# Kernel optimization log

Hardware: AMD Instinct MI355X
Metric: run time of the kernel (lower is better)

Reference implementation:

```python
import jax, jax.numpy as jnp
import numpy as np

N = 50000      # nodes
E = 800000     # edges (avg degree 16)
F = 6          # input node features
C = 64         # conv_hidden_channels
M = 256        # mlp_hidden_channels
NCLS = 24      # num_classes
EPS = 1e-5     # BatchNorm eps


def _bn(h, g, b):
    # BatchNorm1d in training mode: biased batch stats over the batch axis
    mu = h.mean(axis=0)
    var = ((h - mu) ** 2).mean(axis=0)
    return g * (h - mu) * jax.lax.rsqrt(var + EPS) + b


def _block(x, W, b, g, beta):
    # Lin -> ReLU -> BN  (one MLP block)
    return _bn(jax.nn.relu(x @ W + b), g, beta)


def _edge_conv(x, src, dst, Wa, ba, ga, bea, Wb, bb, gb, beb):
    # EdgeConv: message = MLP([x_i, x_j - x_i]), max-aggregated onto target i
    xi = x[dst]                                   # [E, d]
    xj = x[src]                                   # [E, d]
    e = jnp.concatenate([xi, xj - xi], axis=-1)   # [E, 2d]
    h = _block(_block(e, Wa, ba, ga, bea), Wb, bb, gb, beb)  # [E, C]
    agg = jax.ops.segment_max(h, dst, num_segments=N)        # [N, C]
    return jnp.where(jnp.isfinite(agg), agg, 0.0)  # zero-fill isolated nodes


def setup_inputs() -> dict:
    key = jax.random.key(0)
    ks = jax.random.split(key, 12)

    def w(k, shape, fan_in):
        return jax.random.normal(k, shape, jnp.float32) * (1.0 / np.sqrt(fan_in))

    z = lambda *s: jnp.zeros(s, jnp.float32)
    o = lambda *s: jnp.ones(s, jnp.float32)

    x = jax.random.normal(ks[0], (N, F), jnp.float32)
    edge_index = jax.random.randint(ks[1], (2, E), 0, N, jnp.int32)

    return {
        "x": x,
        # conv1 MLP: Lin(2F,C)+BN, Lin(C,C)+BN
        "W1a": w(ks[2], (2 * F, C), 2 * F), "b1a": z(C), "g1a": o(C), "be1a": z(C),
        "W1b": w(ks[3], (C, C), C),         "b1b": z(C), "g1b": o(C), "be1b": z(C),
        # conv2/conv3 stacked: Lin(2C,C)+BN, Lin(C,C)+BN
        "Wa": w(ks[4], (2, 2 * C, C), 2 * C), "ba": z(2, C), "ga": o(2, C), "bea": z(2, C),
        "Wb": w(ks[5], (2, C, C), C),         "bb": z(2, C), "gb": o(2, C), "beb": z(2, C),
        # lin1: Lin(3C, M)+BN
        "Wl": w(ks[6], (3 * C, M), 3 * C), "bl": z(M), "gl": o(M), "bel": z(M),
        # head: Lin(M, M/4)+BN, Lin(M/4, M/8)+BN, Lin(M/8, NCLS)
        "Wm1": w(ks[7], (M, M // 4), M),      "bm1": z(M // 4), "gm1": o(M // 4), "bem1": z(M // 4),
        "Wm2": w(ks[8], (M // 4, M // 8), M // 4), "bm2": z(M // 8), "gm2": o(M // 8), "bem2": z(M // 8),
        "Wo": w(ks[9], (M // 8, NCLS), M // 8), "bo": z(NCLS),
        "edge_index": edge_index,
    }


def reference(x, W1a, b1a, g1a, be1a, W1b, b1b, g1b, be1b,
              Wa, ba, ga, bea, Wb, bb, gb, beb,
              Wl, bl, gl, bel,
              Wm1, bm1, gm1, bem1, Wm2, bm2, gm2, bem2,
              Wo, bo, edge_index):
    src, dst = edge_index[0], edge_index[1]
    x1 = _edge_conv(x,  src, dst, W1a, b1a, g1a, be1a, W1b, b1b, g1b, be1b)
    x2 = _edge_conv(x1, src, dst, Wa[0], ba[0], ga[0], bea[0], Wb[0], bb[0], gb[0], beb[0])
    x3 = _edge_conv(x2, src, dst, Wa[1], ba[1], ga[1], bea[1], Wb[1], bb[1], gb[1], beb[1])
    h = _block(jnp.concatenate([x1, x2, x3], axis=-1), Wl, bl, gl, bel)
    h = _block(h, Wm1, bm1, gm1, bem1)   # Dropout is identity (eval)
    h = _block(h, Wm2, bm2, gm2, bem2)   # Dropout is identity (eval)
    logits = h @ Wo + bo
    return jax.nn.log_softmax(logits, axis=1)
```

## Files before the change

### kernel.cpp

```cpp
#include <hip/hip_runtime.h>
#include <hip/hip_bf16.h>

#define EPS 1e-5f
typedef unsigned short bfr;
typedef unsigned short hfr;
typedef _Float16 h2v __attribute__((ext_vector_type(2)));
typedef _Float16 f16x8 __attribute__((ext_vector_type(8)));
typedef float f32x4 __attribute__((ext_vector_type(4)));

#if defined(__has_builtin)
#if __has_builtin(__builtin_amdgcn_fdot2)
#define HAS_FDOT2 1
#endif
#endif

static inline int cdiv(int a, int b){ return (a + b - 1) / b; }
static inline int imin(int a, int b){ return a < b ? a : b; }

__device__ __forceinline__ float bf2f(bfr u){ return __uint_as_float((unsigned)u << 16); }
__device__ __forceinline__ bfr f2bf(float f){
  unsigned u = __float_as_uint(f);
  u += 0x7fffu + ((u >> 16) & 1u);
  return (bfr)(u >> 16);
}
__device__ __forceinline__ unsigned pack2bf(float a, float b){
  return (unsigned)f2bf(a) | ((unsigned)f2bf(b) << 16);
}
__device__ __forceinline__ float h2f(hfr u){ _Float16 h; __builtin_memcpy(&h, &u, 2); return (float)h; }
__device__ __forceinline__ hfr f2h(float f){ _Float16 h = (_Float16)f; hfr u; __builtin_memcpy(&u, &h, 2); return u; }
__device__ __forceinline__ unsigned pack2h(float a, float b){
  return (unsigned)f2h(a) | ((unsigned)f2h(b) << 16);
}
__device__ __forceinline__ h2v u2h2(unsigned u){ h2v r; __builtin_memcpy(&r, &u, 4); return r; }
__device__ __forceinline__ unsigned h22u(h2v h){ unsigned u; __builtin_memcpy(&u, &h, 4); return u; }
__device__ __forceinline__ float dot2(h2v a, h2v b, float c){
#ifdef HAS_FDOT2
  return __builtin_amdgcn_fdot2(a, b, c, false);
#else
  return c + (float)a.x * (float)b.x + (float)a.y * (float)b.y;
#endif
}

__global__ __launch_bounds__(256) void detect_kernel(const bfr* __restrict__ xr, int nwords, int* __restrict__ flag){
  int i = threadIdx.x;
  int bad = 0;
  if (i < nwords){
    bfr lo = xr[2 * i];
    int e = (lo >> 7) & 0xFF;
    bool plausible = ((lo & 0x7FFF) == 0) || (e >= 97 && e <= 157);
    bad = plausible ? 0 : 1;
  }
  __shared__ int s[256];
  s[threadIdx.x] = bad; __syncthreads();
  for (int st = 128; st; st >>= 1){
    if (threadIdx.x < st) s[threadIdx.x] += s[threadIdx.x + st];
    __syncthreads();
  }
  if (threadIdx.x == 0) *flag = (s[0] > 32) ? 1 : 0;
}

#define NPAR 31
struct ParamPtrs { const void* p[NPAR]; };
struct ParamOfs  { int off[NPAR + 1]; };

__global__ __launch_bounds__(256) void acvt_batch_kernel(ParamPtrs pp, ParamOfs po,
                                                         float* __restrict__ out, int total,
                                                         const int* __restrict__ flag){
  int g = blockIdx.x * 256 + threadIdx.x;
  if (g >= total) return;
  int isf = *flag;
  int t = 0;
  while (po.off[t + 1] <= g) ++t;
  int i = g - po.off[t];
  out[g] = isf ? ((const float*)pp.p[t])[i] : bf2f(((const bfr*)pp.p[t])[i]);
}

__global__ __launch_bounds__(256) void deg_kernel(const int* __restrict__ dst, int* __restrict__ deg, int E){
  int e = blockIdx.x * 256 + threadIdx.x;
  if (e < E) atomicAdd(&deg[dst[e]], 1);
}

__global__ __launch_bounds__(256) void scan1_kernel(const int* __restrict__ deg, int* __restrict__ locoff,
                                                    int* __restrict__ bsum, int N){
  __shared__ int s[256];
  int i = blockIdx.x * 256 + threadIdx.x;
  int v = (i < N) ? deg[i] : 0;
  s[threadIdx.x] = v; __syncthreads();
  for (int st = 1; st < 256; st <<= 1){
    int u = (threadIdx.x >= st) ? s[threadIdx.x - st] : 0;
    __syncthreads();
    s[threadIdx.x] += u;
    __syncthreads();
  }
  if (i < N) locoff[i] = s[threadIdx.x] - v;
  if (threadIdx.x == 255) bsum[blockIdx.x] = s[255];
}

__global__ __launch_bounds__(256) void scan2_kernel(int* __restrict__ bsum, int nb){
  __shared__ int s[256];
  const int t = threadIdx.x;
  int carry = 0;
  for (int base = 0; base < nb; base += 256){
    int v = (base + t < nb) ? bsum[base + t] : 0;
    s[t] = v; __syncthreads();
    for (int st = 1; st < 256; st <<= 1){
      int u = (t >= st) ? s[t - st] : 0;
      __syncthreads();
      s[t] += u;
      __syncthreads();
    }
    if (base + t < nb) bsum[base + t] = carry + s[t] - v;
    carry += s[255];
    __syncthreads();
  }
}

__global__ __launch_bounds__(256) void scan3_kernel(const int* __restrict__ locoff, const int* __restrict__ bsum,
                                                    int* __restrict__ row_off, int* __restrict__ cur,
                                                    int N, int E){
  int i = blockIdx.x * 256 + threadIdx.x;
  if (i < N){
    int v = locoff[i] + bsum[blockIdx.x];
    row_off[i] = v; cur[i] = v;
  }
  if (i == 0) row_off[N] = E;
}

__global__ __launch_bounds__(256) void scatter_kernel(const int* __restrict__ src, const int* __restrict__ dst,
                                                      int* __restrict__ cur, int* __restrict__ ssrc, int E){
  int e = blockIdx.x * 256 + threadIdx.x;
  if (e < E){
    int d = dst[e];
    int p = atomicAdd(&cur[d], 1);
    ssrc[p] = src[e];
  }
}

template<bool FIRST>
__global__ __launch_bounds__(256) void gemmPQ_kernel(const void* __restrict__ Av, int lda,
                                                     const float* __restrict__ Wa, int d,
                                                     const float* __restrict__ ba,
                                                     hfr* __restrict__ P, hfr* __restrict__ Q, int N){
  __shared__ unsigned WsU[64 * 64];
  const int y = blockIdx.y;
  const int tot = d * 64;
  if (FIRST){
    float* Ws = (float*)WsU;
    for (int i = threadIdx.x; i < tot; i += 256)
      Ws[i] = y ? Wa[tot + i] : (Wa[i] - Wa[tot + i]);
  } else {
    for (int i = threadIdx.x; i < 32 * 64; i += 256){
      int p = i >> 6, c = i & 63;
      int i0 = (2 * p) * 64 + c, i1 = (2 * p + 1) * 64 + c;
      float w0 = y ? Wa[tot + i0] : (Wa[i0] - Wa[tot + i0]);
      float w1 = y ? Wa[tot + i1] : (Wa[i1] - Wa[tot + i1]);
      WsU[i] = pack2h(w0, w1);
    }
  }
  __syncthreads();
  const int row = blockIdx.x * 256 + threadIdx.x;
  if (row >= N) return;
  float acc[64];
#pragma unroll
  for (int c = 0; c < 64; ++c) acc[c] = 0.f;
  if (FIRST){
    const float* Ws = (const float*)WsU;
    const float* Af = (const float*)Av + (size_t)row * lda;
    for (int k = 0; k < d; ++k){
      float a = Af[k];
      const float* wr = Ws + k * 64;
#pragma unroll
      for (int c4 = 0; c4 < 16; ++c4){
        float4 w = *(const float4*)(wr + 4 * c4);
        acc[4*c4+0] += a * w.x; acc[4*c4+1] += a * w.y;
        acc[4*c4+2] += a * w.z; acc[4*c4+3] += a * w.w;
      }
    }
  } else {
    const hfr* Ah = (const hfr*)Av + (size_t)row * lda;
#pragma unroll
    for (int k8 = 0; k8 < 8; ++k8){
      uint4 av = *(const uint4*)(Ah + k8 * 8);
      unsigned pr[4] = {av.x, av.y, av.z, av.w};
#pragma unroll
      for (int pi = 0; pi < 4; ++pi){
        h2v ap = u2h2(pr[pi]);
        const unsigned* wr = WsU + (k8 * 4 + pi) * 64;
#pragma unroll
        for (int c = 0; c < 64; ++c) acc[c] = dot2(ap, u2h2(wr[c]), acc[c]);
      }
    }
  }
  if (!y){
#pragma unroll
    for (int c = 0; c < 64; ++c) acc[c] += ba[c];
  }
  unsigned p[32];
#pragma unroll
  for (int c = 0; c < 64; c += 2) p[c / 2] = pack2h(acc[c], acc[c + 1]);
  hfr* outp = (y ? Q : P) + (size_t)row * 64;
  uint4* op = (uint4*)outp;
#pragma unroll
  for (int i = 0; i < 8; ++i) op[i] = make_uint4(p[4*i], p[4*i+1], p[4*i+2], p[4*i+3]);
}

template<int NOUT, int KSTEPS, bool FOLD, bool PQ, bool STATS>
__global__ __launch_bounds__(256) void mgemm_kernel(const hfr* __restrict__ Ah, int lda,
                                                    const float* __restrict__ Wp0, const float* __restrict__ Wm0, int ldw,
                                                    const float* __restrict__ bias0,
                                                    const float* __restrict__ stats, float cntInv,
                                                    const float* __restrict__ g, const float* __restrict__ be,
                                                    hfr* __restrict__ Ov0, hfr* __restrict__ Ov1, int ldo,
                                                    float* __restrict__ statsOut, int statC,
                                                    int nrows, int relu){
  constexpr int K  = KSTEPS * 32;
  constexpr int KP = K + 8;
  constexpr int NT = NOUT / 16;
  __shared__ __align__(16) _Float16 W2T[NOUT * KP];
  __shared__ __align__(16) _Float16 etile[4][16][NOUT + 8];
  __shared__ float aS[FOLD ? K : 1], bbS[FOLD ? K : 1], bsum[FOLD ? 256 : 1];
  __shared__ float bfull[NOUT];
  __shared__ float sred[STATS ? 4 * NOUT : 1], qred[STATS ? 4 * NOUT : 1];
  const int tid = threadIdx.x;
  const int lane = tid & 63;
  const int wib = tid >> 6;
  const float* Wp = Wp0;
  const float* Wm = Wm0;
  const float* bias = bias0;
  hfr* Ov = Ov0;
  int colbase = blockIdx.y * NOUT;
  if (PQ){
    colbase = 0;
    if (blockIdx.y == 1){ Wp = Wp0 + (size_t)K * ldw; Wm = nullptr; bias = nullptr; Ov = Ov1; }
    else { Wm = Wp0 + (size_t)K * ldw; }
  }

  if (FOLD){
    for (int k = tid; k < K; k += 256){
      float mu = stats[k] * cntInv;
      float var = stats[K + k] * cntInv - mu * mu;
      float ai = g[k] * rsqrtf(var + EPS);
      aS[k] = ai; bbS[k] = be[k] - ai * mu;
    }
    __syncthreads();
  }
  for (int i = tid; i < K * NOUT; i += 256){
    int k = i / NOUT, c = i - k * NOUT;
    float w = Wp[(size_t)k * ldw + colbase + c];
    if (Wm) w -= Wm[(size_t)k * ldw + colbase + c];
    if (FOLD) w *= aS[k];
    W2T[c * KP + k] = (_Float16)w;
  }
  if (FOLD){
    constexpr int parts = 256 / NOUT;
    int c = tid % NOUT, p = tid / NOUT;
    float s = 0.f;
    for (int k = p; k < K; k += parts) s += bbS[k] * Wp[(size_t)k * ldw + colbase + c];
    bsum[p * NOUT + c] = s;
    __syncthreads();
    if (tid < NOUT){
      float t = bias[colbase + tid];
#pragma unroll
      for (int pp = 0; pp < parts; ++pp) t += bsum[pp * NOUT + tid];
      bfull[tid] = t;
    }
  } else {
    if (tid < NOUT) bfull[tid] = bias ? bias[colbase + tid] : 0.f;
  }
  __syncthreads();

  f16x8 Bf[KSTEPS][NT];
#pragma unroll
  for (int s = 0; s < KSTEPS; ++s)
#pragma unroll
    for (int t = 0; t < NT; ++t)
      Bf[s][t] = *(const f16x8*)&W2T[(t * 16 + (lane & 15)) * KP + s * 32 + (lane >> 4) * 8];
  float bc[NT];
#pragma unroll
  for (int t = 0; t < NT; ++t) bc[t] = bfull[t * 16 + (lane & 15)];

  float ssum[STATS ? NT : 1], qsum[STATS ? NT : 1];
  if (STATS){
#pragma unroll
    for (int t = 0; t < (STATS ? NT : 1); ++t){ ssum[t] = 0.f; qsum[t] = 0.f; }
  }
  const int lq2 = lane >> 4;

  const int ntiles = (nrows + 63) >> 6;
  for (int tile = blockIdx.x; tile < ntiles; tile += gridDim.x){
    const int r0 = tile * 64 + wib * 16;
    const int rowA = min(r0 + (lane & 15), nrows - 1);
    const hfr* Ap = Ah + (size_t)rowA * lda + (lane >> 4) * 8;
    f32x4 acc[NT];
#pragma unroll
    for (int t = 0; t < NT; ++t) acc[t] = (f32x4){bc[t], bc[t], bc[t], bc[t]};
#pragma unroll
    for (int s = 0; s < KSTEPS; ++s){
      f16x8 Af = *(const f16x8*)(Ap + s * 32);
#pragma unroll
      for (int t = 0; t < NT; ++t)
        acc[t] = __builtin_amdgcn_mfma_f32_16x16x32_f16(Af, Bf[s][t], acc[t], 0, 0, 0);
    }
    const bool fullTile = (r0 + 16 <= nrows);
#pragma unroll
    for (int t = 0; t < NT; ++t){
#pragma unroll
      for (int r = 0; r < 4; ++r){
        float v = acc[t][r];
        v = relu ? fmaxf(v, 0.f) : v;
        if (STATS){
          float vs = v;
          if (!fullTile) vs = ((r0 + lq2 * 4 + r) < nrows) ? vs : 0.f;
          ssum[t] += vs;
          qsum[t]  = fmaf(vs, vs, qsum[t]);
        }
        etile[wib][lq2 * 4 + r][t * 16 + (lane & 15)] = (_Float16)v;
      }
    }
    if (NOUT == 64){
#pragma unroll
      for (int h = 0; h < 2; ++h){
        int rl = h * 8 + (lane >> 3);
        int ch = lane & 7;
        uint4 vv = *(const uint4*)&etile[wib][rl][ch * 8];
        int rg = r0 + rl;
        if (rg < nrows) *(uint4*)(Ov + (size_t)rg * ldo + colbase + ch * 8) = vv;
      }
    } else {
      int rl = lane >> 2;
      int ch = lane & 3;
      uint4 vv = *(const uint4*)&etile[wib][rl][ch * 8];
      int rg = r0 + rl;
      if (rg < nrows) *(uint4*)(Ov + (size_t)rg * ldo + colbase + ch * 8) = vv;
    }
  }

  if (STATS){
#pragma unroll
    for (int t = 0; t < NT; ++t){
      float s = ssum[t], q = qsum[t];
      s += __shfl_xor(s, 16, 64); s += __shfl_xor(s, 32, 64);
      q += __shfl_xor(q, 16, 64); q += __shfl_xor(q, 32, 64);
      if (lq2 == 0){ sred[wib * NOUT + t * 16 + lane] = s; qred[wib * NOUT + t * 16 + lane] = q; }
    }
    __syncthreads();
    if (tid < NOUT){
      float s = sred[tid] + sred[NOUT + tid] + sred[2 * NOUT + tid] + sred[3 * NOUT + tid];
      float q = qred[tid] + qred[NOUT + tid] + qred[2 * NOUT + tid] + qred[3 * NOUT + tid];
      atomicAdd(&statsOut[colbase + tid], s);
      atomicAdd(&statsOut[statC + colbase + tid], q);
    }
  }
}

__global__ __launch_bounds__(256) void passA_kernel(const hfr* __restrict__ P, const hfr* __restrict__ Q,
                                                    const int* __restrict__ ssrc, const int* __restrict__ row_off,
                                                    float* __restrict__ stats, hfr* __restrict__ h1, int N){
  const int tid = threadIdx.x;
  const int lane = tid & 63;
  const int wib = tid >> 6;
  const int er0 = lane >> 3;
  const int ck = lane & 7;
  const int wid = (blockIdx.x * 256 + tid) >> 6;
  const int nw = (gridDim.x * 256) >> 6;
  const _Float16 z16 = (_Float16)0;
  float s8[8], q8[8];
#pragma unroll
  for (int j = 0; j < 8; ++j){ s8[j] = 0.f; q8[j] = 0.f; }
  for (int n = wid; n < N; n += nw){
    const int e0 = row_off[n], e1 = row_off[n + 1];
    if (e0 >= e1) continue;
    uint4 pv4 = ((const uint4*)(P + (size_t)n * 64))[ck];
    h2v pp0 = u2h2(pv4.x), pp1 = u2h2(pv4.y), pp2 = u2h2(pv4.z), pp3 = u2h2(pv4.w);
    const int lim = e1 - 1;
    for (int eb = e0; eb < e1; eb += 16){
      int sv = ssrc[min(eb + (lane & 15), lim)];
#pragma unroll
      for (int h = 0; h < 2; ++h){
        int er = h * 8 + er0;
        int ge = eb + er;
        int sj = __shfl(sv, er, 64);
        uint4 qv = *((const uint4*)(Q + (size_t)sj * 64) + ck);
        h2v s0 = u2h2(qv.x) + pp0;
        h2v s1 = u2h2(qv.y) + pp1;
        h2v s2 = u2h2(qv.z) + pp2;
        h2v s3 = u2h2(qv.w) + pp3;
        s0.x = (s0.x < z16) ? z16 : s0.x; s0.y = (s0.y < z16) ? z16 : s0.y;
        s1.x = (s1.x < z16) ? z16 : s1.x; s1.y = (s1.y < z16) ? z16 : s1.y;
        s2.x = (s2.x < z16) ? z16 : s2.x; s2.y = (s2.y < z16) ? z16 : s2.y;
        s3.x = (s3.x < z16) ? z16 : s3.x; s3.y = (s3.y < z16) ? z16 : s3.y;
        if (ge < e1){
          *(uint4*)(h1 + (size_t)ge * 64 + ck * 8) = make_uint4(h22u(s0), h22u(s1), h22u(s2), h22u(s3));
          float v;
          v = (float)s0.x; s8[0] += v; q8[0] = fmaf(v, v, q8[0]);
          v = (float)s0.y; s8[1] += v; q8[1] = fmaf(v, v, q8[1]);
          v = (float)s1.x; s8[2] += v; q8[2] = fmaf(v, v, q8[2]);
          v = (float)s1.y; s8[3] += v; q8[3] = fmaf(v, v, q8[3]);
          v = (float)s2.x; s8[4] += v; q8[4] = fmaf(v, v, q8[4]);
          v = (float)s2.y; s8[5] += v; q8[5] = fmaf(v, v, q8[5]);
          v = (float)s3.x; s8[6] += v; q8[6] = fmaf(v, v, q8[6]);
          v = (float)s3.y; s8[7] += v; q8[7] = fmaf(v, v, q8[7]);
        }
      }
    }
  }
#pragma unroll
  for (int j = 0; j < 8; ++j){
    float s = s8[j], q = q8[j];
    s += __shfl_xor(s, 8, 64);  q += __shfl_xor(q, 8, 64);
    s += __shfl_xor(s, 16, 64); q += __shfl_xor(q, 16, 64);
    s += __shfl_xor(s, 32, 64); q += __shfl_xor(q, 32, 64);
    s8[j] = s; q8[j] = q;
  }
  __shared__ float ls[4][64], lq[4][64];
  if (lane < 8){
#pragma unroll
    for (int j = 0; j < 8; ++j){ ls[wib][lane * 8 + j] = s8[j]; lq[wib][lane * 8 + j] = q8[j]; }
  }
  __syncthreads();
  if (tid < 64){
    atomicAdd(&stats[tid], ls[0][tid] + ls[1][tid] + ls[2][tid] + ls[3][tid]);
  } else if (tid < 128){
    int c = tid - 64;
    atomicAdd(&stats[64 + c], lq[0][c] + lq[1][c] + lq[2][c] + lq[3][c]);
  }
}

__global__ __launch_bounds__(256) void passBC_kernel(const hfr* __restrict__ h1,
                                                     const int* __restrict__ row_off,
                                                     const float* __restrict__ statsIn, float Einv,
                                                     const float* __restrict__ g1, const float* __restrict__ be1,
                                                     const float* __restrict__ Wb, const float* __restrict__ bn,
                                                     float* __restrict__ agg, float* __restrict__ statsOut, int N){
  __shared__ __align__(16) _Float16 W2T[64 * 72];
  __shared__ float aS[64], bbS[64], b2S[64], bsum[256], qsum[256];
  const int tid = threadIdx.x;
  const int lane = tid & 63;
  if (tid < 64){
    float mu = statsIn[tid] * Einv;
    float var = statsIn[64 + tid] * Einv - mu * mu;
    float ai = g1[tid] * rsqrtf(var + EPS);
    aS[tid] = ai; bbS[tid] = be1[tid] - ai * mu;
  }
  __syncthreads();
  for (int i = tid; i < 4096; i += 256){
    int c = i >> 6, k = i & 63;
    W2T[c * 72 + k] = (_Float16)(aS[k] * Wb[(size_t)k * 64 + c]);
  }
  {
    int c = tid & 63, p = tid >> 6;
    float s = 0.f;
    for (int k = p; k < 64; k += 4) s += bbS[k] * Wb[(size_t)k * 64 + c];
    bsum[p * 64 + c] = s;
  }
  __syncthreads();
  if (tid < 64) b2S[tid] = bn[tid] + bsum[tid] + bsum[64 + tid] + bsum[128 + tid] + bsum[192 + tid];
  __syncthreads();
  f16x8 Bf[4][2];
#pragma unroll
  for (int t = 0; t < 4; ++t)
#pragma unroll
    for (int h = 0; h < 2; ++h){
      int c = t * 16 + (lane & 15);
      Bf[t][h] = *(const f16x8*)&W2T[c * 72 + h * 32 + (lane >> 4) * 8];
    }
  float bc[4];
#pragma unroll
  for (int t = 0; t < 4; ++t) bc[t] = b2S[t * 16 + (lane & 15)];
  const int wid = (blockIdx.x * 256 + tid) >> 6;
  const int nw = (gridDim.x * 256) >> 6;
  float sumT[4] = {0.f,0.f,0.f,0.f}, sqT[4] = {0.f,0.f,0.f,0.f};
  for (int n = wid; n < N; n += nw){
    const int e0 = row_off[n], e1 = row_off[n + 1];
    if (e0 >= e1) continue;
    float mxT[4] = {0.f,0.f,0.f,0.f};
    for (int eb = e0; eb < e1; eb += 16){
      const hfr* ap = h1 + (size_t)(eb + (lane & 15)) * 64 + (lane >> 4) * 8;
      f16x8 A0 = *(const f16x8*)ap;
      f16x8 A1 = *(const f16x8*)(ap + 32);
#pragma unroll
      for (int t = 0; t < 4; ++t){
        f32x4 Cv = {bc[t], bc[t], bc[t], bc[t]};
        Cv = __builtin_amdgcn_mfma_f32_16x16x32_f16(A0, Bf[t][0], Cv, 0, 0, 0);
        Cv = __builtin_amdgcn_mfma_f32_16x16x32_f16(A1, Bf[t][1], Cv, 0, 0, 0);
#pragma unroll
        for (int r = 0; r < 4; ++r){
          int rowi = (lane >> 4) * 4 + r;
          float v = fmaxf(Cv[r], 0.f);
          v = ((eb + rowi) < e1) ? v : 0.f;
          mxT[t] = fmaxf(mxT[t], v);
          sumT[t] += v;
          sqT[t]  = fmaf(v, v, sqT[t]);
        }
      }
    }
#pragma unroll
    for (int t = 0; t < 4; ++t){
      float m = mxT[t];
      m = fmaxf(m, __shfl_xor(m, 16, 64));
      m = fmaxf(m, __shfl_xor(m, 32, 64));
      mxT[t] = m;
    }
    float outv = (lane < 16) ? mxT[0] : (lane < 32) ? mxT[1] : (lane < 48) ? mxT[2] : mxT[3];
    agg[(size_t)n * 64 + lane] = outv;
  }
#pragma unroll
  for (int t = 0; t < 4; ++t){
    float s = sumT[t], q = sqT[t];
    s += __shfl_xor(s, 16, 64); s += __shfl_xor(s, 32, 64);
    q += __shfl_xor(q, 16, 64); q += __shfl_xor(q, 32, 64);
    sumT[t] = s; sqT[t] = q;
  }
  float ssel = (lane < 16) ? sumT[0] : (lane < 32) ? sumT[1] : (lane < 48) ? sumT[2] : sumT[3];
  float qsel = (lane < 16) ? sqT[0]  : (lane < 32) ? sqT[1]  : (lane < 48) ? sqT[2]  : sqT[3];
  bsum[tid] = ssel; qsum[tid] = qsel;
  __syncthreads();
  if (tid < 64){
    atomicAdd(&statsOut[tid], bsum[tid] + bsum[64 + tid] + bsum[128 + tid] + bsum[192 + tid]);
  } else if (tid < 128){
    int c = tid - 64;
    atomicAdd(&statsOut[64 + c], qsum[c] + qsum[64 + c] + qsum[128 + c] + qsum[192 + c]);
  }
}

__global__ __launch_bounds__(256) void fixup_kernel(const float* __restrict__ agg, const int* __restrict__ deg,
                                                    const float* __restrict__ stats, float cntInv,
                                                    const float* __restrict__ g, const float* __restrict__ be,
                                                    hfr* __restrict__ xout, int ldx, int N){
  int t = blockIdx.x * 256 + threadIdx.x;
  if (t >= N * 64) return;
  int n = t >> 6, c = t & 63;
  float mu = stats[c] * cntInv;
  float var = stats[64 + c] * cntInv - mu * mu;
  float a = g[c] * rsqrtf(var + EPS);
  float b = be[c] - a * mu;
  float v = 0.f;
  if (deg[n] > 0) v = a * agg[t] + b;
  xout[(size_t)n * ldx + c] = f2h(v);
}

__global__ __launch_bounds__(256) void head_kernel(const hfr* __restrict__ u2,
                                                   const float* __restrict__ stats, float cntInv,
                                                   const float* __restrict__ g, const float* __restrict__ be,
                                                   const float* __restrict__ Wo, const float* __restrict__ bo,
                                                   void* __restrict__ out, int N, const int* __restrict__ flag){
  __shared__ float Ws[32 * 24];
  __shared__ float bs[24];
  __shared__ float aS[32], bbS[32];
  const int tid = threadIdx.x;
  if (tid < 32){
    float mu = stats[tid] * cntInv;
    float var = stats[32 + tid] * cntInv - mu * mu;
    float ai = g[tid] * rsqrtf(var + EPS);
    aS[tid] = ai; bbS[tid] = be[tid] - ai * mu;
  }
  __syncthreads();
  for (int i = tid; i < 32 * 24; i += 256){
    int k = i / 24, c = i - 24 * k;
    Ws[i] = aS[k] * Wo[(size_t)k * 24 + c];
  }
  if (tid < 24){
    float t = bo[tid];
    for (int k = 0; k < 32; ++k) t += bbS[k] * Wo[(size_t)k * 24 + tid];
    bs[tid] = t;
  }
  __syncthreads();
  int r = blockIdx.x * 256 + tid;
  if (r >= N) return;
  int isf = *flag;
  float l[24];
#pragma unroll
  for (int c = 0; c < 24; ++c) l[c] = bs[c];
  const hfr* up = u2 + (size_t)r * 32;
#pragma unroll
  for (int k = 0; k < 32; ++k){
    float v = h2f(up[k]);
#pragma unroll
    for (int c = 0; c < 24; ++c) l[c] += v * Ws[k * 24 + c];
  }
  float m = l[0];
#pragma unroll
  for (int c = 1; c < 24; ++c) m = fmaxf(m, l[c]);
  float s = 0.f;
#pragma unroll
  for (int c = 0; c < 24; ++c) s += expf(l[c] - m);
  float lse = m + logf(s);
  if (isf){
    float4* op = (float4*)((float*)out + (size_t)r * 24);
#pragma unroll
    for (int i = 0; i < 6; ++i)
      op[i] = make_float4(l[4*i] - lse, l[4*i+1] - lse, l[4*i+2] - lse, l[4*i+3] - lse);
  } else {
    unsigned p[12];
#pragma unroll
    for (int c = 0; c < 24; c += 2) p[c / 2] = pack2bf(l[c] - lse, l[c + 1] - lse);
    uint4* op = (uint4*)((bfr*)out + (size_t)r * 24);
#pragma unroll
    for (int i = 0; i < 3; ++i) op[i] = make_uint4(p[4*i], p[4*i+1], p[4*i+2], p[4*i+3]);
  }
}

extern "C" void kernel_launch(void* const* d_in, const int* in_sizes, int n_in,
                              void* d_out, int out_size, void* d_ws, size_t ws_size,
                              hipStream_t stream){
  const int N = in_sizes[0] / 6;
  const int E = in_sizes[31] / 2;
  const int* edge = (const int*)d_in[31];
  const int* src = edge;
  const int* dst = edge + E;

  size_t off = 0; char* basep = (char*)d_ws;
  auto alloc = [&](size_t bytes) -> void* {
    void* p = basep + off;
    off = (off + bytes + 255) & ~(size_t)255;
    return p;
  };
  float* stA  = (float*)alloc(1472 * 4);
  float* stN1 = stA + 768;
  float* stN2 = stA + 1280;
  float* stN3 = stA + 1408;
  int*   flag = (int*)  alloc(4);
  int*   deg  = (int*)  alloc((size_t)N * 4);
  int*   rowo = (int*)  alloc((size_t)(N + 1) * 4);
  int*   cur  = (int*)  alloc((size_t)N * 4);
  int*   loco = (int*)  alloc((size_t)N * 4);
  int*   bsc  = (int*)  alloc(1024 * 4);
  int*   ssrc = (int*)  alloc((size_t)E * 4);

  ParamPtrs pp; ParamOfs po;
  int hoff[32]; int total = 0;
  for (int s = 0; s < NPAR; ++s){
    int idx = (s < 30) ? (s + 1) : 0;
    pp.p[s] = d_in[idx];
    po.off[s] = total;
    hoff[idx] = total;
    total += in_sizes[idx];
  }
  po.off[NPAR] = total;
  float* pf = (float*)alloc((size_t)total * 4);

  hfr*   P    = (hfr*)  alloc((size_t)N * 64 * 2);
  hfr*   Qb   = (hfr*)  alloc((size_t)N * 64 * 2);
  float* agg  = (float*)alloc((size_t)N * 64 * 4);
  hfr*   xcat = (hfr*)  alloc((size_t)N * 192 * 2);
  hfr*   h1   = (hfr*)  alloc((size_t)(E + 16) * 64 * 2);
  hfr* u_l = (hfr*)P;
  hfr* u1  = xcat;
  hfr* u2  = xcat + (size_t)N * 64;
  (void)ws_size; (void)n_in; (void)out_size;

  dim3 B(256);
  detect_kernel<<<1, B, 0, stream>>>((const bfr*)d_in[0], 256, flag);
  acvt_batch_kernel<<<cdiv(total, 256), B, 0, stream>>>(pp, po, pf, total, flag);

  hipMemsetAsync(stA, 0, 1472 * 4, stream);
  hipMemsetAsync(deg, 0, (size_t)N * 4, stream);
  hipMemsetAsync(h1 + (size_t)E * 64, 0, 16 * 64 * 2, stream);
  deg_kernel<<<cdiv(E, 256), B, 0, stream>>>(dst, deg, E);
  const int NBn = cdiv(N, 256);
  scan1_kernel<<<NBn, B, 0, stream>>>(deg, loco, bsc, N);
  scan2_kernel<<<1, B, 0, stream>>>(bsc, NBn);
  scan3_kernel<<<NBn, B, 0, stream>>>(loco, bsc, rowo, cur, N, E);
  scatter_kernel<<<cdiv(E, 256), B, 0, stream>>>(src, dst, cur, ssrc, E);

  const int NB = cdiv(N, 256);
  const int ntiles = cdiv(N, 64);
  const int GWA = 1024, GWB = 1024;
  const float Einv = 1.f / (float)E;
  for (int k = 0; k < 3; ++k){
    const float *Wa_k, *ba_k, *ga_k, *bea_k, *Wb_k, *bb_k, *gb_k, *beb_k;
    if (k == 0){
      Wa_k = pf + hoff[1]; ba_k = pf + hoff[2]; ga_k = pf + hoff[3]; bea_k = pf + hoff[4];
      Wb_k = pf + hoff[5]; bb_k = pf + hoff[6]; gb_k = pf + hoff[7]; beb_k = pf + hoff[8];
    } else {
      int kk = k - 1;
      Wa_k = pf + hoff[9]  + (size_t)kk * 128 * 64;
      ba_k = pf + hoff[10] + kk * 64;
      ga_k = pf + hoff[11] + kk * 64;
      bea_k= pf + hoff[12] + kk * 64;
      Wb_k = pf + hoff[13] + (size_t)kk * 64 * 64;
      bb_k = pf + hoff[14] + kk * 64;
      gb_k = pf + hoff[15] + kk * 64;
      beb_k= pf + hoff[16] + kk * 64;
    }
    float* st1 = stA + k * 256;
    float* st2 = st1 + 128;
    if (k == 0){
      gemmPQ_kernel<true><<<dim3(NB, 2), B, 0, stream>>>(pf + hoff[0], 6, Wa_k, 6, ba_k, P, Qb, N);
    } else {
      mgemm_kernel<64, 2, false, true, false><<<dim3(imin(ntiles, 1024), 2), B, 0, stream>>>(
          xcat + (size_t)(k - 1) * 64, 192, Wa_k, nullptr, 64, ba_k,
          nullptr, 0.f, nullptr, nullptr, P, Qb, 64, nullptr, 0, N, 0);
    }
    passA_kernel<<<GWA, B, 0, stream>>>(P, Qb, ssrc, rowo, st1, h1, N);
    passBC_kernel<<<GWB, B, 0, stream>>>(h1, rowo, st1, Einv, ga_k, bea_k, Wb_k, bb_k,
                                         agg, st2, N);
    fixup_kernel<<<cdiv(N * 64, 256), B, 0, stream>>>(agg, deg, st2, Einv, gb_k, beb_k,
                                                      xcat + (size_t)k * 64, 192, N);
  }

  mgemm_kernel<64, 6, false, false, true><<<dim3(imin(ntiles, 256), 4), B, 0, stream>>>(
      xcat, 192, pf + hoff[17], nullptr, 256, pf + hoff[18],
      nullptr, 0.f, nullptr, nullptr, u_l, nullptr, 256, stN1, 256, N, 1);
  mgemm_kernel<32, 8, true, false, true><<<dim3(imin(ntiles, 512), 2), B, 0, stream>>>(
      u_l, 256, pf + hoff[21], nullptr, 64, pf + hoff[22],
      stN1, 1.f / (float)N, pf + hoff[19], pf + hoff[20], u1, nullptr, 64, stN2, 64, N, 1);
  mgemm_kernel<32, 2, true, false, true><<<dim3(imin(ntiles, 1024), 1), B, 0, stream>>>(
      u1, 64, pf + hoff[25], nullptr, 32, pf + hoff[26],
      stN2, 1.f / (float)N, pf + hoff[23], pf + hoff[24], u2, nullptr, 32, stN3, 32, N, 1);
  head_kernel<<<cdiv(N, 256), B, 0, stream>>>(u2, stN3, 1.f / (float)N, pf + hoff[27], pf + hoff[28],
                                              pf + hoff[29], pf + hoff[30], d_out, N, flag);
  (void)NB;
}
```

Measured before the change: 723.5 us.

## Fuse scan passes, merge P/Q GEMM into one 128-wide pass, vectorize fixup

Drops the single-block scan2 kernel; each scan3 block now computes its own carry by reducing the preceding block sums. The P and Q projections for conv2/3 are computed in one mgemm launch with NOUT=128, so the A tile is read once instead of twice, and the output is split between the two buffers on write. The fixup kernel now precomputes the BN scale and shift per block in shared memory and handles four channels per thread with float4 loads and packed half stores. These target launch overhead and redundant memory traffic, in exchange for redundant carry sums in scan3 and more weight registers in the wider GEMM.

```diff
diff --git a/kernel.cpp b/kernel.cpp
--- a/kernel.cpp
+++ b/kernel.cpp
@@ -96,31 +96,26 @@
   if (threadIdx.x == 255) bsum[blockIdx.x] = s[255];
 }
 
-__global__ __launch_bounds__(256) void scan2_kernel(int* __restrict__ bsum, int nb){
-  __shared__ int s[256];
-  const int t = threadIdx.x;
-  int carry = 0;
-  for (int base = 0; base < nb; base += 256){
-    int v = (base + t < nb) ? bsum[base + t] : 0;
-    s[t] = v; __syncthreads();
-    for (int st = 1; st < 256; st <<= 1){
-      int u = (t >= st) ? s[t - st] : 0;
-      __syncthreads();
-      s[t] += u;
-      __syncthreads();
-    }
-    if (base + t < nb) bsum[base + t] = carry + s[t] - v;
-    carry += s[255];
-    __syncthreads();
-  }
-}
-
 __global__ __launch_bounds__(256) void scan3_kernel(const int* __restrict__ locoff, const int* __restrict__ bsum,
                                                     int* __restrict__ row_off, int* __restrict__ cur,
                                                     int N, int E){
-  int i = blockIdx.x * 256 + threadIdx.x;
+  __shared__ int s[256];
+  const int t = threadIdx.x;
+  const int bid = blockIdx.x;
+  int acc = 0;
+  for (int base = 0; base < bid; base += 256){
+    int idx = base + t;
+    acc += (idx < bid) ? bsum[idx] : 0;
+  }
+  s[t] = acc; __syncthreads();
+  for (int st = 128; st; st >>= 1){
+    if (t < st) s[t] += s[t + st];
+    __syncthreads();
+  }
+  const int carry = s[0];
+  int i = bid * 256 + t;
   if (i < N){
-    int v = locoff[i] + bsum[blockIdx.x];
+    int v = locoff[i] + carry;
     row_off[i] = v; cur[i] = v;
   }
   if (i == 0) row_off[N] = E;
@@ -204,7 +199,7 @@
   for (int i = 0; i < 8; ++i) op[i] = make_uint4(p[4*i], p[4*i+1], p[4*i+2], p[4*i+3]);
 }
 
-template<int NOUT, int KSTEPS, bool FOLD, bool PQ, bool STATS>
+template<int NOUT, int KSTEPS, bool FOLD, bool PQ, bool STATS, bool PQ2>
 __global__ __launch_bounds__(256) void mgemm_kernel(const hfr* __restrict__ Ah, int lda,
                                                     const float* __restrict__ Wp0, const float* __restrict__ Wm0, int ldw,
                                                     const float* __restrict__ bias0,
@@ -234,6 +229,7 @@
     if (blockIdx.y == 1){ Wp = Wp0 + (size_t)K * ldw; Wm = nullptr; bias = nullptr; Ov = Ov1; }
     else { Wm = Wp0 + (size_t)K * ldw; }
   }
+  if (PQ2) colbase = 0;
 
   if (FOLD){
     for (int k = tid; k < K; k += 256){
@@ -246,8 +242,14 @@
   }
   for (int i = tid; i < K * NOUT; i += 256){
     int k = i / NOUT, c = i - k * NOUT;
-    float w = Wp[(size_t)k * ldw + colbase + c];
-    if (Wm) w -= Wm[(size_t)k * ldw + colbase + c];
+    float w;
+    if (PQ2){
+      w = (c < 64) ? (Wp[(size_t)k * ldw + c] - Wp[(size_t)(K + k) * ldw + c])
+                   : Wp[(size_t)(K + k) * ldw + (c - 64)];
+    } else {
+      w = Wp[(size_t)k * ldw + colbase + c];
+      if (Wm) w -= Wm[(size_t)k * ldw + colbase + c];
+    }
     if (FOLD) w *= aS[k];
     W2T[c * KP + k] = (_Float16)w;
   }
@@ -265,7 +267,11 @@
       bfull[tid] = t;
     }
   } else {
-    if (tid < NOUT) bfull[tid] = bias ? bias[colbase + tid] : 0.f;
+    if (tid < NOUT){
+      float bb = 0.f;
+      if (bias && (!PQ2 || tid < 64)) bb = bias[colbase + tid];
+      bfull[tid] = bb;
+    }
   }
   __syncthreads();
 
@@ -317,7 +323,19 @@
         etile[wib][lq2 * 4 + r][t * 16 + (lane & 15)] = (_Float16)v;
       }
     }
-    if (NOUT == 64){
+    if (PQ2){
+#pragma unroll
+      for (int hh = 0; hh < 4; ++hh){
+        int rl = hh * 4 + (lane >> 4);
+        int ch16 = lane & 15;
+        uint4 vv = *(const uint4*)&etile[wib][rl][ch16 * 8];
+        int rg = r0 + rl;
+        if (rg < nrows){
+          hfr* bp = (ch16 < 8) ? Ov : Ov1;
+          *(uint4*)(bp + (size_t)rg * ldo + (ch16 & 7) * 8) = vv;
+        }
+      }
+    } else if (NOUT == 64){
 #pragma unroll
       for (int h = 0; h < 2; ++h){
         int rl = h * 8 + (lane >> 3);
@@ -527,16 +545,25 @@
                                                     const float* __restrict__ stats, float cntInv,
                                                     const float* __restrict__ g, const float* __restrict__ be,
                                                     hfr* __restrict__ xout, int ldx, int N){
-  int t = blockIdx.x * 256 + threadIdx.x;
-  if (t >= N * 64) return;
-  int n = t >> 6, c = t & 63;
-  float mu = stats[c] * cntInv;
-  float var = stats[64 + c] * cntInv - mu * mu;
-  float a = g[c] * rsqrtf(var + EPS);
-  float b = be[c] - a * mu;
-  float v = 0.f;
-  if (deg[n] > 0) v = a * agg[t] + b;
-  xout[(size_t)n * ldx + c] = f2h(v);
+  __shared__ float aC[64], bC[64];
+  const int tid = threadIdx.x;
+  if (tid < 64){
+    float mu = stats[tid] * cntInv;
+    float var = stats[64 + tid] * cntInv - mu * mu;
+    float a = g[tid] * rsqrtf(var + EPS);
+    aC[tid] = a; bC[tid] = be[tid] - a * mu;
+  }
+  __syncthreads();
+  int t = blockIdx.x * 256 + tid;
+  if (t >= N * 16) return;
+  int n = t >> 4, c4 = (t & 15) * 4;
+  float4 v4 = *(const float4*)(agg + (size_t)n * 64 + c4);
+  bool live = deg[n] > 0;
+  float o0 = live ? fmaf(v4.x, aC[c4 + 0], bC[c4 + 0]) : 0.f;
+  float o1 = live ? fmaf(v4.y, aC[c4 + 1], bC[c4 + 1]) : 0.f;
+  float o2 = live ? fmaf(v4.z, aC[c4 + 2], bC[c4 + 2]) : 0.f;
+  float o3 = live ? fmaf(v4.w, aC[c4 + 3], bC[c4 + 3]) : 0.f;
+  *(uint2*)(xout + (size_t)n * ldx + c4) = make_uint2(pack2h(o0, o1), pack2h(o2, o3));
 }
 
 __global__ __launch_bounds__(256) void head_kernel(const hfr* __restrict__ u2,
@@ -659,7 +686,6 @@
   deg_kernel<<<cdiv(E, 256), B, 0, stream>>>(dst, deg, E);
   const int NBn = cdiv(N, 256);
   scan1_kernel<<<NBn, B, 0, stream>>>(deg, loco, bsc, N);
-  scan2_kernel<<<1, B, 0, stream>>>(bsc, NBn);
   scan3_kernel<<<NBn, B, 0, stream>>>(loco, bsc, rowo, cur, N, E);
   scatter_kernel<<<cdiv(E, 256), B, 0, stream>>>(src, dst, cur, ssrc, E);
 
@@ -688,24 +714,24 @@
     if (k == 0){
       gemmPQ_kernel<true><<<dim3(NB, 2), B, 0, stream>>>(pf + hoff[0], 6, Wa_k, 6, ba_k, P, Qb, N);
     } else {
-      mgemm_kernel<64, 2, false, true, false><<<dim3(imin(ntiles, 1024), 2), B, 0, stream>>>(
+      mgemm_kernel<128, 2, false, false, false, true><<<dim3(imin(ntiles, 1024), 1), B, 0, stream>>>(
           xcat + (size_t)(k - 1) * 64, 192, Wa_k, nullptr, 64, ba_k,
           nullptr, 0.f, nullptr, nullptr, P, Qb, 64, nullptr, 0, N, 0);
     }
     passA_kernel<<<GWA, B, 0, stream>>>(P, Qb, ssrc, rowo, st1, h1, N);
     passBC_kernel<<<GWB, B, 0, stream>>>(h1, rowo, st1, Einv, ga_k, bea_k, Wb_k, bb_k,
                                          agg, st2, N);
-    fixup_kernel<<<cdiv(N * 64, 256), B, 0, stream>>>(agg, deg, st2, Einv, gb_k, beb_k,
+    fixup_kernel<<<cdiv(N * 16, 256), B, 0, stream>>>(agg, deg, st2, Einv, gb_k, beb_k,
                                                       xcat + (size_t)k * 64, 192, N);
   }
 
-  mgemm_kernel<64, 6, false, false, true><<<dim3(imin(ntiles, 256), 4), B, 0, stream>>>(
+  mgemm_kernel<64, 6, false, false, true, false><<<dim3(imin(ntiles, 256), 4), B, 0, stream>>>(
       xcat, 192, pf + hoff[17], nullptr, 256, pf + hoff[18],
       nullptr, 0.f, nullptr, nullptr, u_l, nullptr, 256, stN1, 256, N, 1);
-  mgemm_kernel<32, 8, true, false, true><<<dim3(imin(ntiles, 512), 2), B, 0, stream>>>(
+  mgemm_kernel<32, 8, true, false, true, false><<<dim3(imin(ntiles, 512), 2), B, 0, stream>>>(
       u_l, 256, pf + hoff[21], nullptr, 64, pf + hoff[22],
       stN1, 1.f / (float)N, pf + hoff[19], pf + hoff[20], u1, nullptr, 64, stN2, 64, N, 1);
-  mgemm_kernel<32, 2, true, false, true><<<dim3(imin(ntiles, 1024), 1), B, 0, stream>>>(
+  mgemm_kernel<32, 2, true, false, true, false><<<dim3(imin(ntiles, 1024), 1), B, 0, stream>>>(
       u1, 64, pf + hoff[25], nullptr, 32, pf + hoff[26],
       stN2, 1.f / (float)N, pf + hoff[23], pf + hoff[24], u2, nullptr, 32, stN3, 32, N, 1);
   head_kernel<<<cdiv(N, 256), B, 0, stream>>>(u2, stN3, 1.f / (float)N, pf + hoff[27], pf + hoff[28],
```

Measured after the change: 737.6 us. About the same (+2.0%).
